# Kernel optimization log

Measured on AMD Instinct MI355X. Metric: run time of the kernel, lower is better.

The kernel has to match this reference:

```python
import jax, jax.numpy as jnp
import numpy as np

B, L, N = 8, 5, 4096
RADIUS, K = 0.7, 32
SPATIAL_STRIDE = 16
TK, TSTRIDE = 3, 2  # temporal kernel / stride; temporal_padding=[1,1] replicate
DIM, DEPTH, HEADS, DIM_HEAD, MLP_DIM, OUT_DIM = 512, 5, 8, 64, 1024, 1088
INNER = HEADS * DIM_HEAD
N_ANCH = 64
NTOT = N + N_ANCH
M = NTOT // SPATIAL_STRIDE  # spatial anchors per output frame


def setup_inputs() -> dict:
    key = jax.random.key(0)
    ks = list(jax.random.split(key, 16))
    s = 0.02
    p = {}
    p["points"] = jax.random.uniform(ks[0], (B, L, N, 3), jnp.float32, -1.0, 1.0)
    p["conv_d_w"] = jax.random.normal(ks[1], (DIM, 4), jnp.float32) * s
    p["conv_f_w"] = jax.random.normal(ks[2], (DIM, 3), jnp.float32) * s
    p["pos_w"] = jax.random.normal(ks[3], (DIM, 4), jnp.float32) * s
    p["pos_b"] = jnp.zeros((DIM,), jnp.float32)
    p["ln1_g"] = jnp.ones((DEPTH, DIM)); p["ln1_b"] = jnp.zeros((DEPTH, DIM))
    p["qkv_w"] = jax.random.normal(ks[4], (DEPTH, DIM, 3 * INNER), jnp.float32) * s
    p["attn_out_w"] = jax.random.normal(ks[5], (DEPTH, INNER, DIM), jnp.float32) * s
    p["attn_out_b"] = jnp.zeros((DEPTH, DIM))
    p["ln2_g"] = jnp.ones((DEPTH, DIM)); p["ln2_b"] = jnp.zeros((DEPTH, DIM))
    p["ff1_w"] = jax.random.normal(ks[6], (DEPTH, DIM, MLP_DIM), jnp.float32) * s
    p["ff1_b"] = jnp.zeros((DEPTH, MLP_DIM))
    p["ff2_w"] = jax.random.normal(ks[7], (DEPTH, MLP_DIM, DIM), jnp.float32) * s
    p["ff2_b"] = jnp.zeros((DEPTH, DIM))
    p["head_ln_g"] = jnp.ones((DIM,)); p["head_ln_b"] = jnp.zeros((DIM,))
    p["head1_w"] = jax.random.normal(ks[8], (DIM, MLP_DIM), jnp.float32) * s
    p["head1_b"] = jnp.zeros((MLP_DIM,))
    p["head2_w"] = jax.random.normal(ks[9], (MLP_DIM, OUT_DIM), jnp.float32) * s
    p["head2_b"] = jnp.zeros((OUT_DIM,))
    return p


def _layer_norm(x, g, b, eps=1e-5):
    mu = jnp.mean(x, -1, keepdims=True)
    var = jnp.mean((x - mu) ** 2, -1, keepdims=True)
    return (x - mu) * jax.lax.rsqrt(var + eps) * g + b


def _anchor_grid():
    lin = jnp.linspace(-1.5, 1.5, 4)
    gx, gy, gz = jnp.meshgrid(lin, lin, lin, indexing="ij")
    return jnp.stack([gx.ravel(), gy.ravel(), gz.ravel()], -1)  # (64,3)


def _fps(pts, m):
    # furthest point sampling, pts (N,3) -> (m,) int32, first pick is index 0 (pointnet2 semantics)
    def step(carry, _):
        dist, last = carry
        d = jnp.sum((pts - pts[last]) ** 2, -1)
        dist = jnp.minimum(dist, d)
        return (dist, jnp.argmax(dist).astype(jnp.int32)), last
    init = (jnp.full((pts.shape[0],), 1e10, pts.dtype), jnp.int32(0))
    _, idx = jax.lax.scan(step, init, None, length=m)
    return idx


def _ball_query(anchors, pts, radius, k):
    # first k point indices within radius of each anchor; pad with first hit (0 if none)
    d2 = jnp.sum((anchors[:, None, :] - pts[None, :, :]) ** 2, -1)  # (M,N)
    n = pts.shape[0]
    cand = jnp.where(d2 < radius * radius, jnp.arange(n, dtype=jnp.int32), n)
    neg_topk, _ = jax.lax.top_k(-cand, k)  # k smallest indices, ascending
    idx = -neg_topk
    first = idx[:, :1]
    idx = jnp.where(idx == n, first, idx)
    return jnp.where(idx == n, 0, idx)


def _forward(points, conv_d_w, conv_f_w, pos_w, pos_b, ln1_g, ln1_b, qkv_w,
             attn_out_w, attn_out_b, ln2_g, ln2_b, ff1_w, ff1_b, ff2_w, ff2_b,
             head_ln_g, head_ln_b, head1_w, head1_b, head2_w, head2_b):
    anch = _anchor_grid()  # (64,3)
    pts = jnp.concatenate(
        [points[..., :3], jnp.broadcast_to(anch, (B, L, N_ANCH, 3))], axis=2)  # (B,L,NTOT,3)
    # replicate temporal padding [1,1]
    frames = jnp.concatenate([pts[:, :1], pts, pts[:, -1:]], axis=1)  # (B,L+2,NTOT,3)

    trad = (TK - 1) // 2
    nT = L + 2
    gather = jax.vmap(lambda p, i: p[i])
    out_xyz, out_feat = [], []
    for t in range(trad, nT - trad, TSTRIDE):
        f_t = frames[:, t]                                   # (B,NTOT,3)
        a_idx = jax.vmap(lambda p: _fps(p, M))(f_t)          # (B,M)
        a_xyz = gather(f_t, a_idx)                           # (B,M,3)
        feats_w = []
        for i in range(t - trad, t + trad + 1):
            nb = frames[:, i]                                # (B,NTOT,3)
            idx = jax.vmap(lambda a, p: _ball_query(a, p, RADIUS, K))(a_xyz, nb)  # (B,M,K)
            grouped = gather(nb, idx)                        # (B,M,K,3)
            disp = grouped - a_xyz[:, :, None, :]
            tdisp = jnp.full((B, M, K, 1), float(i - t), disp.dtype)
            disp4 = jnp.concatenate([disp, tdisp], -1)       # (B,M,K,4)
            # conv_f(features) + conv_d(displacement); features fed in are the xyz themselves
            feat = (jnp.einsum("bmkc,dc->bmkd", grouped, conv_f_w)
                    + jnp.einsum("bmkc,dc->bmkd", disp4, conv_d_w))
            feats_w.append(jnp.max(feat, axis=2))            # spatial max -> (B,M,DIM)
        out_feat.append(jnp.max(jnp.stack(feats_w, 0), axis=0))  # temporal max
        out_xyz.append(a_xyz)

    nF = len(out_xyz)
    xyzs = jnp.stack(out_xyz, 1)                             # (B,nF,M,3)
    feats = jnp.stack(out_feat, 1).reshape(B, nF * M, DIM)
    tcol = jnp.broadcast_to(
        jnp.arange(1, nF + 1, dtype=xyzs.dtype)[None, :, None, None], (B, nF, M, 1))
    xyzts = jnp.concatenate([xyzs, tcol], -1).reshape(B, nF * M, 4)
    x = jnp.einsum("bnc,dc->bnd", xyzts, pos_w) + pos_b + feats  # (B,T,DIM); emb_relu=False

    scale = DIM_HEAD ** -0.5
    for l in range(DEPTH):
        xn = _layer_norm(x, ln1_g[l], ln1_b[l])
        q, k, v = jnp.split(xn @ qkv_w[l], 3, axis=-1)
        rs = lambda a: a.reshape(B, -1, HEADS, DIM_HEAD)
        q, k, v = rs(q), rs(k), rs(v)
        att = jax.nn.softmax(jnp.einsum("bqhd,bkhd->bhqk", q, k) * scale, axis=-1)
        o = jnp.einsum("bhqk,bkhd->bqhd", att, v).reshape(B, -1, INNER)
        x = x + o @ attn_out_w[l] + attn_out_b[l]
        xn = _layer_norm(x, ln2_g[l], ln2_b[l])
        x = x + jax.nn.gelu(xn @ ff1_w[l] + ff1_b[l], approximate=False) @ ff2_w[l] + ff2_b[l]

    x = jnp.max(x, axis=1)                                   # (B,DIM)
    x = _layer_norm(x, head_ln_g, head_ln_b)
    x = jax.nn.gelu(x @ head1_w + head1_b, approximate=False) @ head2_w + head2_b
    x = x.reshape(B, 1, OUT_DIM // 64, 64)
    x = jax.nn.softmax(x, axis=-1)
    return x @ anch                                          # (B,1,J,3)


def reference(points, conv_d_w, conv_f_w, pos_w, pos_b, ln1_g, ln1_b, qkv_w,
              attn_out_w, attn_out_b, ln2_g, ln2_b, ff1_w, ff1_b, ff2_w, ff2_b,
              head_ln_g, head_ln_b, head1_w, head1_b, head2_w, head2_b):
    return _forward(points, conv_d_w, conv_f_w, pos_w, pos_b, ln1_g, ln1_b, qkv_w,
                    attn_out_w, attn_out_b, ln2_g, ln2_b, ff1_w, ff1_b, ff2_w, ff2_b,
                    head_ln_g, head_ln_b, head1_w, head1_b, head2_w, head2_b)
```

## Files before the change

kernel.cpp:

```cpp
#include <hip/hip_runtime.h>
#include <hip/hip_bf16.h>
#include <cstddef>

#define BB 8
#define LL 5
#define NN 4096
#define NANCH 64
#define NPTS 4160
#define MM 260
#define NFRAME 3
#define SSEQ 780
#define DIMC 512
#define NHEAD 8
#define DHEAD 64
#define MLPD 1024
#define OUTD 1088
#define NROWS 6240
#define VPITCH 784
#define WBUFSZ 2097152

typedef __attribute__((ext_vector_type(8))) short s16x8;
typedef __attribute__((ext_vector_type(4))) float fx4;
typedef unsigned short ushort_t;
typedef unsigned int uint_t;

__device__ __forceinline__ float sqdist_rn(float x1, float y1, float z1,
                                           float x2, float y2, float z2) {
    float dx = __fsub_rn(x1, x2);
    float dy = __fsub_rn(y1, y2);
    float dz = __fsub_rn(z1, z2);
    return __fadd_rn(__fadd_rn(__fmul_rn(dx, dx), __fmul_rn(dy, dy)), __fmul_rn(dz, dz));
}

__device__ __forceinline__ float gelu_exact(float v) {
    return 0.5f * v * (1.0f + erff(v * 0.70710678118654752440f));
}

__device__ __forceinline__ uint_t bf16rn(float f) {
    uint_t u = __float_as_uint(f);
    return (u + 0x7FFFu + ((u >> 16) & 1u)) >> 16;
}
__device__ __forceinline__ void split2(float f, ushort_t& h, ushort_t& l) {
    uint_t hb = bf16rn(f);
    h = (ushort_t)hb;
    float fh = __uint_as_float(hb << 16);
    l = (ushort_t)bf16rn(f - fh);
}

typedef __attribute__((address_space(3))) unsigned int as3u;
typedef const __attribute__((address_space(1))) unsigned int as1u;
__device__ __forceinline__ void gload16(const ushort_t* g, ushort_t* l) {
    __builtin_amdgcn_global_load_lds((as1u*)g, (as3u*)l, 16, 0, 0);
}

template <int CTRL>
__device__ __forceinline__ int dpp_mov(int v) {
    return __builtin_amdgcn_update_dpp(0, v, CTRL, 0xF, 0xF, true);
}
#define DPP_STEP_F(op, v, ctrl) v = op(v, __int_as_float(dpp_mov<ctrl>(__float_as_int(v))))
__device__ __forceinline__ float wave_max_bcast(float v) {
    DPP_STEP_F(fmaxf, v, 0x111); DPP_STEP_F(fmaxf, v, 0x112);
    DPP_STEP_F(fmaxf, v, 0x114); DPP_STEP_F(fmaxf, v, 0x118);
    DPP_STEP_F(fmaxf, v, 0x142); DPP_STEP_F(fmaxf, v, 0x143);
    return __int_as_float(__builtin_amdgcn_readlane(__float_as_int(v), 63));
}
__device__ __forceinline__ float faddf(float a, float b) { return a + b; }
__device__ __forceinline__ float wave_sum_bcast(float v) {
    DPP_STEP_F(faddf, v, 0x111); DPP_STEP_F(faddf, v, 0x112);
    DPP_STEP_F(faddf, v, 0x114); DPP_STEP_F(faddf, v, 0x118);
    DPP_STEP_F(faddf, v, 0x142); DPP_STEP_F(faddf, v, 0x143);
    return __int_as_float(__builtin_amdgcn_readlane(__float_as_int(v), 63));
}
__device__ __forceinline__ float row16_maxf(float v) {
    DPP_STEP_F(fmaxf, v, 0x111); DPP_STEP_F(fmaxf, v, 0x112);
    DPP_STEP_F(fmaxf, v, 0x114); DPP_STEP_F(fmaxf, v, 0x118);
    return __int_as_float(__builtin_amdgcn_readlane(__float_as_int(v), 15));
}

__device__ __forceinline__ void wsplit_tile(
    int bid, int tid, int nthr,
    const float* __restrict__ qkvw, const float* __restrict__ projw,
    const float* __restrict__ ff1w, const float* __restrict__ ff2w,
    ushort_t* __restrict__ th, ushort_t* __restrict__ tl,
    float (*T)[33]) {
    const float* src; int K, N; size_t dst;
    if (bid < 768)       { src = qkvw;  K = 512;  N = 1536; dst = 0;       }
    else if (bid < 1024) { src = projw; K = 512;  N = 512;  dst = 786432;  bid -= 768;  }
    else if (bid < 1536) { src = ff1w;  K = 512;  N = 1024; dst = 1048576; bid -= 1024; }
    else                 { src = ff2w;  K = 1024; N = 512;  dst = 1572864; bid -= 1536; }
    int ntn = N >> 5;
    int tn = bid % ntn, tk = bid / ntn;
    int n0 = tn * 32, k0 = tk * 32;
    for (int e = tid; e < 1024; e += nthr) {
        int r = e >> 5, c = e & 31;
        T[r][c] = src[(size_t)(k0 + r) * N + n0 + c];
    }
    __syncthreads();
    for (int e = tid; e < 1024; e += nthr) {
        int r = e >> 5, c = e & 31;
        ushort_t h, l;
        split2(T[c][r], h, l);
        th[dst + (size_t)(n0 + r) * K + k0 + c] = h;
        tl[dst + (size_t)(n0 + r) * K + k0 + c] = l;
    }
}

__global__ __launch_bounds__(256) void build_pts_kernel(const float* __restrict__ points,
                                                        float* __restrict__ pts) {
    int i = blockIdx.x * 256 + threadIdx.x;
    if (i >= BB * LL * NPTS) return;
    int n = i % NPTS;
    int bl = i / NPTS;
    if (n < NN) {
        const float* src = points + ((size_t)bl * NN + n) * 3;
        pts[(size_t)i * 3 + 0] = src[0];
        pts[(size_t)i * 3 + 1] = src[1];
        pts[(size_t)i * 3 + 2] = src[2];
    } else {
        int j = n - NN;
        int ix = j >> 4, iy = (j >> 2) & 3, iz = j & 3;
        pts[(size_t)i * 3 + 0] = -1.5f + (float)ix;
        pts[(size_t)i * 3 + 1] = -1.5f + (float)iy;
        pts[(size_t)i * 3 + 2] = -1.5f + (float)iz;
    }
}

__global__ __launch_bounds__(1024) void fps_ws_kernel(
    const float* __restrict__ pts, float* __restrict__ axyz,
    const float* __restrict__ qkvw, const float* __restrict__ projw,
    const float* __restrict__ ff1w, const float* __restrict__ ff2w,
    ushort_t* __restrict__ th, ushort_t* __restrict__ tl) {
    __shared__ __align__(16) char smem[50432];
    int bid = blockIdx.x;
    int tid = threadIdx.x;
    if (bid >= 24) {
        wsplit_tile(bid - 24, tid, 1024, qkvw, projw, ff1w, ff2w, th, tl,
                    (float(*)[33])smem);
        return;
    }
    float* sx = (float*)smem;
    float* sy = sx + NPTS;
    float* sz = sy + NPTS;
    float* redv = sz + NPTS;
    int* redi = (int*)(redv + 32);

    int b = bid / 3, f = bid % 3;
    const float* P = pts + (size_t)(b * LL + 2 * f) * NPTS * 3;
    int lane = tid & 63, wid = tid >> 6;
    int start = tid < 64 ? 5 * tid : 320 + 4 * (tid - 64);
    int cnt = tid < 64 ? 5 : 4;
    float px[5], py[5], pz[5], dist[5];
#pragma unroll
    for (int j = 0; j < 5; j++) {
        if (j < cnt) {
            int n = start + j;
            float gx = P[(size_t)n * 3 + 0];
            float gy = P[(size_t)n * 3 + 1];
            float gz = P[(size_t)n * 3 + 2];
            px[j] = gx; py[j] = gy; pz[j] = gz;
            sx[n] = gx; sy[n] = gy; sz[n] = gz;
            dist[j] = 1e10f;
        } else {
            px[j] = 0.f; py[j] = 0.f; pz[j] = 0.f;
            dist[j] = -1.0f;
        }
    }
    __syncthreads();
    float ax = sx[0], ay = sy[0], az = sz[0];
    float* out = axyz + (size_t)bid * MM * 3;
    for (int m = 0; m < MM; m++) {
        if (tid == 0) { out[m * 3 + 0] = ax; out[m * 3 + 1] = ay; out[m * 3 + 2] = az; }
        float bv = -1.0f;
#pragma unroll
        for (int j = 0; j < 4; j++) {
            float d = sqdist_rn(px[j], py[j], pz[j], ax, ay, az);
            float dj = fminf(dist[j], d);
            dist[j] = dj;
            bv = fmaxf(bv, dj);
        }
        if (cnt == 5) {
            float d = sqdist_rn(px[4], py[4], pz[4], ax, ay, az);
            float dj = fminf(dist[4], d);
            dist[4] = dj;
            bv = fmaxf(bv, dj);
        }
        float wmv = wave_max_bcast(bv);
        unsigned long long mk = __ballot(bv == wmv);
        int srcl = __ffsll(mk) - 1;
        int fn = start;
#pragma unroll
        for (int j = 4; j >= 0; j--)
            if (dist[j] == wmv) fn = start + j;
        int wn = __builtin_amdgcn_readlane(fn, srcl);
        int par = (m & 1) * 16;
        if (lane == 0) { redv[par + wid] = wmv; redi[par + wid] = wn; }
        __syncthreads();
        float cv = redv[par + (lane & 15)];
        int ci = redi[par + (lane & 15)];
        float bw = row16_maxf(cv);
        unsigned long long mk2 = __ballot(cv == bw);
        int w16 = __ffsll(mk2) - 1;
        int bn = __builtin_amdgcn_readlane(ci, w16);
        ax = sx[bn]; ay = sy[bn]; az = sz[bn];
    }
}

__global__ __launch_bounds__(64) void group_conv_kernel(
    const float* __restrict__ pts, const float* __restrict__ axyz,
    const float* __restrict__ conv_d_w, const float* __restrict__ conv_f_w,
    const float* __restrict__ pos_w, const float* __restrict__ pos_b,
    float* __restrict__ x) {
    int gid = blockIdx.x;
    int b = gid / SSEQ;
    int rem = gid % SSEQ;
    int f = rem / MM;
    int lane = threadIdx.x;
    const float* A = axyz + (size_t)gid * 3;
    float ax = A[0], ay = A[1], az = A[2];

    float cf0[8], cf1[8], cf2[8], cd0[8], cd1[8], cd2[8], cd3[8], fmx[8];
#pragma unroll
    for (int c = 0; c < 8; c++) {
        int d = lane + 64 * c;
        cf0[c] = conv_f_w[d * 3 + 0];
        cf1[c] = conv_f_w[d * 3 + 1];
        cf2[c] = conv_f_w[d * 3 + 2];
        cd0[c] = conv_d_w[d * 4 + 0];
        cd1[c] = conv_d_w[d * 4 + 1];
        cd2[c] = conv_d_w[d * 4 + 2];
        cd3[c] = conv_d_w[d * 4 + 3];
        fmx[c] = -INFINITY;
    }
    __shared__ int nbr[32];
    __shared__ float gxs[32], gys[32], gzs[32];
    const float R2 = 0.49000000953674316f;

    for (int wi = 0; wi < 3; wi++) {
        int l = 2 * f + wi - 1;
        l = l < 0 ? 0 : (l > 4 ? 4 : l);
        const float* P = pts + (size_t)(b * LL + l) * NPTS * 3;
        int cnt = 0;
        for (int base = 0; base < NPTS && cnt < 32; base += 64) {
            int n = base + lane;
            float d2 = sqdist_rn(P[(size_t)n * 3], P[(size_t)n * 3 + 1], P[(size_t)n * 3 + 2],
                                 ax, ay, az);
            bool hit = d2 < R2;
            unsigned long long mk = __ballot(hit);
            int rank = (int)__popcll(mk & (((unsigned long long)1 << lane) - 1ull));
            if (hit && (cnt + rank) < 32) nbr[cnt + rank] = n;
            cnt += (int)__popcll(mk);
        }
        __syncthreads();
        int eff = cnt < 32 ? cnt : 32;
        if (lane < 32) {
            int idx = (eff == 0) ? 0 : (lane < eff ? nbr[lane] : nbr[0]);
            gxs[lane] = P[(size_t)idx * 3 + 0];
            gys[lane] = P[(size_t)idx * 3 + 1];
            gzs[lane] = P[(size_t)idx * 3 + 2];
        }
        __syncthreads();
        float tf = (float)(wi - 1);
        for (int k = 0; k < 32; k++) {
            float gx = gxs[k], gy = gys[k], gz = gzs[k];
            float dx = gx - ax, dy = gy - ay, dz = gz - az;
#pragma unroll
            for (int c = 0; c < 8; c++) {
                float v = gx * cf0[c] + gy * cf1[c] + gz * cf2[c] +
                          dx * cd0[c] + dy * cd1[c] + dz * cd2[c] + tf * cd3[c];
                fmx[c] = fmaxf(fmx[c], v);
            }
        }
        __syncthreads();
    }
    float tcol = (float)(f + 1);
#pragma unroll
    for (int c = 0; c < 8; c++) {
        int d = lane + 64 * c;
        float pos = ax * pos_w[d * 4 + 0] + ay * pos_w[d * 4 + 1] +
                    az * pos_w[d * 4 + 2] + tcol * pos_w[d * 4 + 3] + pos_b[d];
        x[(size_t)gid * DIMC + d] = fmx[c] + pos;
    }
}

__global__ __launch_bounds__(64) void ln_kernel(const float* __restrict__ x,
                                                const float* __restrict__ g,
                                                const float* __restrict__ b,
                                                ushort_t* __restrict__ yh,
                                                ushort_t* __restrict__ yl) {
    int r = blockIdx.x;
    int lane = threadIdx.x;
    const float* xr = x + (size_t)r * DIMC;
    float4 v0 = *(const float4*)(xr + lane * 8);
    float4 v1 = *(const float4*)(xr + lane * 8 + 4);
    float s = v0.x + v0.y + v0.z + v0.w + v1.x + v1.y + v1.z + v1.w;
    s = wave_sum_bcast(s);
    float mean = s * (1.0f / 512.0f);
    float dv[8];
    dv[0] = v0.x - mean; dv[1] = v0.y - mean; dv[2] = v0.z - mean; dv[3] = v0.w - mean;
    dv[4] = v1.x - mean; dv[5] = v1.y - mean; dv[6] = v1.z - mean; dv[7] = v1.w - mean;
    float sq = 0.f;
#pragma unroll
    for (int c = 0; c < 8; c++) sq += dv[c] * dv[c];
    sq = wave_sum_bcast(sq);
    float var = sq * (1.0f / 512.0f);
    float inv = 1.0f / sqrtf(var + 1e-5f);
    int d = lane * 8;
    ushort_t hs[8], ls[8];
#pragma unroll
    for (int c = 0; c < 8; c++) {
        float v = dv[c] * inv * g[d + c] + b[d + c];
        split2(v, hs[c], ls[c]);
    }
    uint4 hv, lv;
    hv.x = hs[0] | ((uint_t)hs[1] << 16); hv.y = hs[2] | ((uint_t)hs[3] << 16);
    hv.z = hs[4] | ((uint_t)hs[5] << 16); hv.w = hs[6] | ((uint_t)hs[7] << 16);
    lv.x = ls[0] | ((uint_t)ls[1] << 16); lv.y = ls[2] | ((uint_t)ls[3] << 16);
    lv.z = ls[4] | ((uint_t)ls[5] << 16); lv.w = ls[6] | ((uint_t)ls[7] << 16);
    *(uint4*)(yh + (size_t)r * DIMC + d) = hv;
    *(uint4*)(yl + (size_t)r * DIMC + d) = lv;
}

#define BK 32

template <int BN, int EPI>
__global__ __launch_bounds__(256) void gemm_mfma(
    const ushort_t* __restrict__ Ahg, const ushort_t* __restrict__ Alg,
    const ushort_t* __restrict__ Bhg, const ushort_t* __restrict__ Blg,
    const float* __restrict__ bias, const float* __restrict__ R,
    float* __restrict__ C, ushort_t* __restrict__ Ch, ushort_t* __restrict__ Cl,
    ushort_t* __restrict__ Vh, ushort_t* __restrict__ Vl,
    int M, int N, int K) {
    const int WN = BN / 2, NT = WN / 16;
    __shared__ __align__(16) ushort_t Ah[128 * BK];
    __shared__ __align__(16) ushort_t Al[128 * BK];
    __shared__ __align__(16) ushort_t Bh[BN * BK];
    __shared__ __align__(16) ushort_t Bl[BN * BK];
    int tid = threadIdx.x;
    int lane = tid & 63, w = tid >> 6;
    int wm = w & 1, wn = w >> 1;
    int quad = lane >> 4, l15 = lane & 15;
    int m0 = blockIdx.y * 128, n0 = blockIdx.x * BN;

    int sr = lane >> 2;
    int sc = lane & 3;
    int kq = ((sc ^ ((sr >> 1) & 3)) << 3);

    int aoff[2];
#pragma unroll
    for (int i = 0; i < 2; i++) {
        int g = w + 4 * i;
        int row = m0 + g * 16 + sr; if (row >= M) row = M - 1;
        aoff[i] = row * K + kq;
    }
    int boff[BN == 128 ? 2 : 1];
    if (BN == 128) {
#pragma unroll
        for (int i = 0; i < 2; i++) {
            int g = w + 4 * i;
            boff[i] = (n0 + g * 16 + sr) * K + kq;
        }
    } else {
        boff[0] = (n0 + w * 16 + sr) * K + kq;
    }

    fx4 acc[4][NT];
#pragma unroll
    for (int mi = 0; mi < 4; mi++)
#pragma unroll
        for (int nj = 0; nj < NT; nj++) acc[mi][nj] = (fx4){0.f, 0.f, 0.f, 0.f};

    int rsw = (l15 >> 1) & 3;
    int aro = (64 * wm + l15) * BK + ((quad ^ rsw) << 3);
    int bro = (WN * wn + l15) * BK + ((quad ^ rsw) << 3);

    for (int k0 = 0; k0 < K; k0 += BK) {
#pragma unroll
        for (int i = 0; i < 2; i++) {
            int g = w + 4 * i;
            gload16(Ahg + aoff[i] + k0, &Ah[g * 16 * BK]);
            gload16(Alg + aoff[i] + k0, &Al[g * 16 * BK]);
        }
        if (BN == 128) {
#pragma unroll
            for (int i = 0; i < 2; i++) {
                int g = w + 4 * i;
                gload16(Bhg + boff[i] + k0, &Bh[g * 16 * BK]);
                gload16(Blg + boff[i] + k0, &Bl[g * 16 * BK]);
            }
        } else {
            gload16(Bhg + boff[0] + k0, &Bh[w * 16 * BK]);
            gload16(Blg + boff[0] + k0, &Bl[w * 16 * BK]);
        }
        __syncthreads();

        s16x8 bf[NT][2];
#pragma unroll
        for (int nj = 0; nj < NT; nj++) {
            bf[nj][0] = *(const s16x8*)&Bh[bro + 16 * nj * BK];
            bf[nj][1] = *(const s16x8*)&Bl[bro + 16 * nj * BK];
        }
#pragma unroll
        for (int mi = 0; mi < 4; mi++) {
            s16x8 aH = *(const s16x8*)&Ah[aro + 16 * mi * BK];
            s16x8 aL = *(const s16x8*)&Al[aro + 16 * mi * BK];
#pragma unroll
            for (int nj = 0; nj < NT; nj++) {
                acc[mi][nj] = __builtin_amdgcn_mfma_f32_16x16x32_bf16(aH, bf[nj][0], acc[mi][nj], 0, 0, 0);
                acc[mi][nj] = __builtin_amdgcn_mfma_f32_16x16x32_bf16(aH, bf[nj][1], acc[mi][nj], 0, 0, 0);
                acc[mi][nj] = __builtin_amdgcn_mfma_f32_16x16x32_bf16(aL, bf[nj][0], acc[mi][nj], 0, 0, 0);
            }
        }
        __syncthreads();
    }
#pragma unroll
    for (int mi = 0; mi < 4; mi++) {
#pragma unroll
        for (int r = 0; r < 4; r++) {
            int row = m0 + 64 * wm + 16 * mi + quad * 4 + r;
            if (row < M) {
#pragma unroll
                for (int nj = 0; nj < NT; nj++) {
                    int col = n0 + WN * wn + 16 * nj + l15;
                    float v = acc[mi][nj][r];
                    if (EPI == 0) {
                        C[(size_t)row * N + col] = v;
                    } else if (EPI == 3) {
                        C[(size_t)row * N + col] = v + bias[col] + R[(size_t)row * N + col];
                    } else if (EPI == 2) {
                        float gv = gelu_exact(v + bias[col]);
                        ushort_t h, l;
                        split2(gv, h, l);
                        Ch[(size_t)row * N + col] = h;
                        Cl[(size_t)row * N + col] = l;
                    } else if (EPI == 5) {
                        ushort_t h, l;
                        split2(v, h, l);
                        if (col < 1024) {
                            Ch[(size_t)row * 1024 + col] = h;
                            Cl[(size_t)row * 1024 + col] = l;
                        } else {
                            int bb = row / SSEQ, key = row % SSEQ;
                            int hh = (col - 1024) >> 6, dd = (col - 1024) & 63;
                            size_t vo = ((size_t)((bb * 8 + hh) * 64 + dd)) * VPITCH + key;
                            Vh[vo] = h;
                            Vl[vo] = l;
                        }
                    }
                }
            }
        }
    }
}

#define AP 72

__global__ __launch_bounds__(256, 2) void attn_mfma_kernel(
    const ushort_t* __restrict__ qkh, const ushort_t* __restrict__ qkl,
    const ushort_t* __restrict__ vth, const ushort_t* __restrict__ vtl,
    ushort_t* __restrict__ oh, ushort_t* __restrict__ ol,
    const float* __restrict__ nqkvw, const float* __restrict__ nprojw,
    const float* __restrict__ nff1w, const float* __restrict__ nff2w,
    ushort_t* __restrict__ nth, ushort_t* __restrict__ ntl) {
    __shared__ __align__(16) char smem[73728];
    if (blockIdx.x >= 13) {
        int widx = (blockIdx.x - 13) * 64 + blockIdx.y * 8 + blockIdx.z;
        wsplit_tile(widx, threadIdx.x, 256, nqkvw, nprojw, nff1w, nff2w,
                    nth, ntl, (float(*)[33])smem);
        return;
    }
    ushort_t* Qh  = (ushort_t*)smem;
    ushort_t* Ql  = Qh + 64 * AP;
    ushort_t* Kh  = Ql + 64 * AP;
    ushort_t* Kl  = Kh + 64 * AP;
    ushort_t* Vth = Kl + 64 * AP;
    ushort_t* Vtl = Vth + 64 * AP;
    ushort_t* Ph  = Vtl + 64 * AP;
    ushort_t* Pl  = Ph + 64 * AP;

    int qt = blockIdx.x, h = blockIdx.y, b = blockIdx.z;
    int tid = threadIdx.x;
    int lane = tid & 63, w = tid >> 6;
    int quad = lane >> 4, l15 = lane & 15;
    int bh = b * 8 + h;

    int q0 = qt * 64;
    int nq = SSEQ - q0; if (nq > 64) nq = 64;

#pragma unroll
    for (int i = 0; i < 2; i++) {
        int t = tid + 256 * i;
        int row = t >> 3, c = (t & 7) * 8;
        int gq = q0 + (row < nq ? row : nq - 1);
        size_t go = (size_t)(b * SSEQ + gq) * 1024 + h * 64 + c;
        *(uint4*)&Qh[row * AP + c] = *(const uint4*)(qkh + go);
        *(uint4*)&Ql[row * AP + c] = *(const uint4*)(qkl + go);
    }

    fx4 accO[4];
#pragma unroll
    for (int dj = 0; dj < 4; dj++) accO[dj] = (fx4){0.f, 0.f, 0.f, 0.f};
    fx4 accL = (fx4){0.f, 0.f, 0.f, 0.f};

    s16x8 ones;
#pragma unroll
    for (int j = 0; j < 8; j++) ones[j] = (short)16256;

    for (int kt = 0; kt < 13; kt++) {
        int k0 = kt * 64;
        int nk = SSEQ - k0; if (nk > 64) nk = 64;
        __syncthreads();
#pragma unroll
        for (int i = 0; i < 2; i++) {
            int t = tid + 256 * i;
            int row = t >> 3, c = (t & 7) * 8;
            int gk = k0 + (row < nk ? row : nk - 1);
            size_t go = (size_t)(b * SSEQ + gk) * 1024 + h * 64 + c;
            *(uint4*)&Kh[row * AP + c] = *(const uint4*)(qkh + go + 512);
            *(uint4*)&Kl[row * AP + c] = *(const uint4*)(qkl + go + 512);
            size_t vo = ((size_t)(bh * 64 + row)) * VPITCH + k0 + c;
            *(uint4*)&Vth[row * AP + c] = *(const uint4*)(vth + vo);
            *(uint4*)&Vtl[row * AP + c] = *(const uint4*)(vtl + vo);
        }
        __syncthreads();

        fx4 accS[4];
#pragma unroll
        for (int nj = 0; nj < 4; nj++) accS[nj] = (fx4){0.f, 0.f, 0.f, 0.f};
#pragma unroll
        for (int ks = 0; ks < 2; ks++) {
            s16x8 aH = *(const s16x8*)&Qh[(16 * w + l15) * AP + 32 * ks + quad * 8];
            s16x8 aL = *(const s16x8*)&Ql[(16 * w + l15) * AP + 32 * ks + quad * 8];
#pragma unroll
            for (int nj = 0; nj < 4; nj++) {
                s16x8 bH = *(const s16x8*)&Kh[(16 * nj + l15) * AP + 32 * ks + quad * 8];
                s16x8 bL = *(const s16x8*)&Kl[(16 * nj + l15) * AP + 32 * ks + quad * 8];
                accS[nj] = __builtin_amdgcn_mfma_f32_16x16x32_bf16(aH, bH, accS[nj], 0, 0, 0);
                accS[nj] = __builtin_amdgcn_mfma_f32_16x16x32_bf16(aH, bL, accS[nj], 0, 0, 0);
                accS[nj] = __builtin_amdgcn_mfma_f32_16x16x32_bf16(aL, bH, accS[nj], 0, 0, 0);
            }
        }
#pragma unroll
        for (int nj = 0; nj < 4; nj++) {
            int key = 16 * nj + l15;
            bool valid = key < nk;
#pragma unroll
            for (int r = 0; r < 4; r++) {
                float s = accS[nj][r] * 0.125f;
                float p = valid ? __expf(s) : 0.f;
                ushort_t hh, ll;
                split2(p, hh, ll);
                int qrow = 16 * w + quad * 4 + r;
                Ph[qrow * AP + key] = hh;
                Pl[qrow * AP + key] = ll;
            }
        }
#pragma unroll
        for (int ks = 0; ks < 2; ks++) {
            s16x8 aPh = *(const s16x8*)&Ph[(16 * w + l15) * AP + 32 * ks + quad * 8];
            s16x8 aPl = *(const s16x8*)&Pl[(16 * w + l15) * AP + 32 * ks + quad * 8];
            accL = __builtin_amdgcn_mfma_f32_16x16x32_bf16(aPh, ones, accL, 0, 0, 0);
            accL = __builtin_amdgcn_mfma_f32_16x16x32_bf16(aPl, ones, accL, 0, 0, 0);
#pragma unroll
            for (int dj = 0; dj < 4; dj++) {
                s16x8 bVh = *(const s16x8*)&Vth[(16 * dj + l15) * AP + 32 * ks + quad * 8];
                s16x8 bVl = *(const s16x8*)&Vtl[(16 * dj + l15) * AP + 32 * ks + quad * 8];
                accO[dj] = __builtin_amdgcn_mfma_f32_16x16x32_bf16(aPh, bVh, accO[dj], 0, 0, 0);
                accO[dj] = __builtin_amdgcn_mfma_f32_16x16x32_bf16(aPh, bVl, accO[dj], 0, 0, 0);
                accO[dj] = __builtin_amdgcn_mfma_f32_16x16x32_bf16(aPl, bVh, accO[dj], 0, 0, 0);
            }
        }
    }
#pragma unroll
    for (int r = 0; r < 4; r++) {
        int lq = 16 * w + quad * 4 + r;
        if (lq < nq) {
            float inv = 1.0f / accL[r];
            size_t base = (size_t)(b * SSEQ + q0 + lq) * DIMC + h * 64 + l15;
#pragma unroll
            for (int dj = 0; dj < 4; dj++) {
                ushort_t hh, ll;
                split2(accO[dj][r] * inv, hh, ll);
                oh[base + 16 * dj] = hh;
                ol[base + 16 * dj] = ll;
            }
        }
    }
}

__global__ __launch_bounds__(512) void pool_max_kernel(const float* __restrict__ x,
                                                       float* __restrict__ partial) {
    int c = blockIdx.x;
    int bb = blockIdx.y;
    int d = threadIdx.x;
    const float* xb = x + ((size_t)(bb * SSEQ + c * 60)) * DIMC + d;
    float m = -INFINITY;
#pragma unroll 4
    for (int s = 0; s < 60; s++) m = fmaxf(m, xb[(size_t)s * DIMC]);
    partial[((size_t)bb * 13 + c) * DIMC + d] = m;
}

__global__ __launch_bounds__(512) void pool_ln_kernel(const float* __restrict__ partial,
                                                      const float* __restrict__ g,
                                                      const float* __restrict__ b,
                                                      float* __restrict__ out) {
    int bb = blockIdx.x;
    int d = threadIdx.x;
    const float* pb = partial + (size_t)bb * 13 * DIMC + d;
    float m = -INFINITY;
#pragma unroll
    for (int c = 0; c < 13; c++) m = fmaxf(m, pb[(size_t)c * DIMC]);
    __shared__ float col[512];
    __shared__ float red[512];
    col[d] = m;
    red[d] = m;
    __syncthreads();
    for (int s = 256; s > 0; s >>= 1) {
        if (d < s) red[d] += red[d + s];
        __syncthreads();
    }
    float mean = red[0] * (1.0f / 512.0f);
    __syncthreads();
    float dv = col[d] - mean;
    red[d] = dv * dv;
    __syncthreads();
    for (int s = 256; s > 0; s >>= 1) {
        if (d < s) red[d] += red[d + s];
        __syncthreads();
    }
    float var = red[0] * (1.0f / 512.0f);
    float inv = 1.0f / sqrtf(var + 1e-5f);
    out[(size_t)bb * DIMC + d] = dv * inv * g[d] + b[d];
}

__global__ __launch_bounds__(256) void head1_kernel(const float* __restrict__ in,
                                                    const float* __restrict__ W,
                                                    const float* __restrict__ bias,
                                                    float* __restrict__ out) {
    int g = blockIdx.x, bb = blockIdx.y;
    int tid = threadIdx.x;
    int c = tid & 63, ks = tid >> 6;
    int col = g * 64 + c;
    __shared__ float xr[512];
    xr[tid] = in[(size_t)bb * 512 + tid];
    xr[tid + 256] = in[(size_t)bb * 512 + tid + 256];
    __syncthreads();
    float acc = 0.f;
    const float* Wc = W + col;
    for (int k = ks * 128; k < ks * 128 + 128; k++)
        acc += xr[k] * Wc[(size_t)k * MLPD];
    __shared__ float red[256];
    red[tid] = acc;
    __syncthreads();
    if (ks == 0) {
        float v = red[c] + red[c + 64] + red[c + 128] + red[c + 192] + bias[col];
        out[(size_t)bb * MLPD + col] = gelu_exact(v);
    }
}

__global__ __launch_bounds__(256) void head2_kernel(const float* __restrict__ in,
                                                    const float* __restrict__ W,
                                                    const float* __restrict__ bias,
                                                    float* __restrict__ out) {
    int g = blockIdx.x, bb = blockIdx.y;
    int tid = threadIdx.x;
    int c = tid & 63, ks = tid >> 6;
    int col = g * 64 + c;
    __shared__ float xr[1024];
    xr[tid] = in[(size_t)bb * 1024 + tid];
    xr[tid + 256] = in[(size_t)bb * 1024 + tid + 256];
    xr[tid + 512] = in[(size_t)bb * 1024 + tid + 512];
    xr[tid + 768] = in[(size_t)bb * 1024 + tid + 768];
    __syncthreads();
    float acc = 0.f;
    const float* Wc = W + col;
    for (int k = ks * 256; k < ks * 256 + 256; k++)
        acc += xr[k] * Wc[(size_t)k * OUTD];
    __shared__ float red[256];
    red[tid] = acc;
    __syncthreads();
    if (ks == 0) {
        out[(size_t)bb * OUTD + col] = red[c] + red[c + 64] + red[c + 128] + red[c + 192] + bias[col];
    }
}

__global__ __launch_bounds__(64) void smax_anchor_kernel(const float* __restrict__ h2,
                                                         float* __restrict__ out) {
    int bb = blockIdx.x / 17;
    int gcol = blockIdx.x % 17;
    int j = threadIdx.x;
    float v = h2[(size_t)bb * OUTD + gcol * 64 + j];
    float mx = wave_max_bcast(v);
    float p = expf(v - mx);
    float sum = wave_sum_bcast(p);
    int ix = j >> 4, iy = (j >> 2) & 3, iz = j & 3;
    float sx = wave_sum_bcast(p * (-1.5f + (float)ix));
    float sy = wave_sum_bcast(p * (-1.5f + (float)iy));
    float sz = wave_sum_bcast(p * (-1.5f + (float)iz));
    if (j == 0) {
        float* o = out + ((size_t)bb * 17 + gcol) * 3;
        o[0] = sx / sum;
        o[1] = sy / sum;
        o[2] = sz / sum;
    }
}

extern "C" void kernel_launch(void* const* d_in, const int* in_sizes, int n_in,
                              void* d_out, int out_size, void* d_ws, size_t ws_size,
                              hipStream_t stream) {
    const float* points     = (const float*)d_in[0];
    const float* conv_d_w   = (const float*)d_in[1];
    const float* conv_f_w   = (const float*)d_in[2];
    const float* pos_w      = (const float*)d_in[3];
    const float* pos_b      = (const float*)d_in[4];
    const float* ln1_g      = (const float*)d_in[5];
    const float* ln1_b      = (const float*)d_in[6];
    const float* qkv_w      = (const float*)d_in[7];
    const float* attn_out_w = (const float*)d_in[8];
    const float* attn_out_b = (const float*)d_in[9];
    const float* ln2_g      = (const float*)d_in[10];
    const float* ln2_b      = (const float*)d_in[11];
    const float* ff1_w      = (const float*)d_in[12];
    const float* ff1_b      = (const float*)d_in[13];
    const float* ff2_w      = (const float*)d_in[14];
    const float* ff2_b      = (const float*)d_in[15];
    const float* head_ln_g  = (const float*)d_in[16];
    const float* head_ln_b  = (const float*)d_in[17];
    const float* head1_w    = (const float*)d_in[18];
    const float* head1_b    = (const float*)d_in[19];
    const float* head2_w    = (const float*)d_in[20];
    const float* head2_b    = (const float*)d_in[21];

    float* ws = (float*)d_ws;
    float* pts    = ws;
    float* axyz   = pts + 499200;
    float* xbuf   = axyz + 18720;
    float* qkvreg = xbuf + 3194880;
    float* pooled = qkvreg + 9601024;
    float* h1     = pooled + 4096;
    float* h2     = h1 + 8192;
    float* fend   = h2 + 8704;
    ushort_t* qkh = (ushort_t*)qkvreg;
    ushort_t* qkl = qkh + 6389760;
    ushort_t* vth = qkl + 6389760;
    ushort_t* vtl = vth + 3211264;
    ushort_t* us   = (ushort_t*)fend;
    ushort_t* xnh  = us;
    ushort_t* xnl  = xnh + 3194880;
    ushort_t* atth = xnl + 3194880;
    ushort_t* attl = atth + 3194880;
    ushort_t* ffhh = attl + 3194880;
    ushort_t* ffhl = ffhh + 6389760;
    ushort_t* wbh  = ffhl + 6389760;
    ushort_t* wbl  = wbh + 2 * WBUFSZ;
    float* ppart = qkvreg;

    build_pts_kernel<<<650, 256, 0, stream>>>(points, pts);
    fps_ws_kernel<<<24 + 2048, 1024, 0, stream>>>(
        pts, axyz, qkv_w, attn_out_w, ff1_w, ff2_w, wbh, wbl);
    group_conv_kernel<<<NROWS, 64, 0, stream>>>(pts, axyz, conv_d_w, conv_f_w,
                                                pos_w, pos_b, xbuf);
    const int MB = (NROWS + 127) / 128;
    for (int l = 0; l < 5; l++) {
        ushort_t* wth = wbh + (size_t)(l & 1) * WBUFSZ;
        ushort_t* wtl = wbl + (size_t)(l & 1) * WBUFSZ;
        ushort_t* nth = wbh + (size_t)((l + 1) & 1) * WBUFSZ;
        ushort_t* ntl = wbl + (size_t)((l + 1) & 1) * WBUFSZ;
        int ln2off = l * 512;
        ln_kernel<<<NROWS, 64, 0, stream>>>(xbuf, ln1_g + ln2off, ln1_b + ln2off, xnh, xnl);
        gemm_mfma<128, 5><<<dim3(1536 / 128, MB), 256, 0, stream>>>(
            xnh, xnl, wth, wtl, nullptr, nullptr, nullptr, qkh, qkl, vth, vtl,
            NROWS, 1536, 512);
        int lnx = l + 1;
        attn_mfma_kernel<<<dim3(l < 4 ? 45 : 13, NHEAD, BB), 256, 0, stream>>>(
            qkh, qkl, vth, vtl, atth, attl,
            l < 4 ? qkv_w + (size_t)lnx * 512 * 1536 : nullptr,
            l < 4 ? attn_out_w + (size_t)lnx * 512 * 512 : nullptr,
            l < 4 ? ff1_w + (size_t)lnx * 512 * 1024 : nullptr,
            l < 4 ? ff2_w + (size_t)lnx * 1024 * 512 : nullptr,
            nth, ntl);
        gemm_mfma<64, 3><<<dim3(512 / 64, MB), 256, 0, stream>>>(
            atth, attl, wth + 786432, wtl + 786432, attn_out_b + ln2off, xbuf,
            xbuf, nullptr, nullptr, nullptr, nullptr, NROWS, 512, 512);
        ln_kernel<<<NROWS, 64, 0, stream>>>(xbuf, ln2_g + ln2off, ln2_b + ln2off, xnh, xnl);
        gemm_mfma<128, 2><<<dim3(1024 / 128, MB), 256, 0, stream>>>(
            xnh, xnl, wth + 1048576, wtl + 1048576, ff1_b + l * 1024, nullptr,
            nullptr, ffhh, ffhl, nullptr, nullptr, NROWS, 1024, 512);
        gemm_mfma<64, 3><<<dim3(512 / 64, MB), 256, 0, stream>>>(
            ffhh, ffhl, wth + 1572864, wtl + 1572864, ff2_b + ln2off, xbuf,
            xbuf, nullptr, nullptr, nullptr, nullptr, NROWS, 512, 1024);
    }
    pool_max_kernel<<<dim3(13, BB), 512, 0, stream>>>(xbuf, ppart);
    pool_ln_kernel<<<BB, 512, 0, stream>>>(ppart, head_ln_g, head_ln_b, pooled);
    head1_kernel<<<dim3(16, BB), 256, 0, stream>>>(pooled, head1_w, head1_b, h1);
    head2_kernel<<<dim3(17, BB), 256, 0, stream>>>(h1, head2_w, head2_b, h2);
    smax_anchor_kernel<<<BB * 17, 64, 0, stream>>>(h2, (float*)d_out);
}
```

Before: 1.987 ms.

## Shrink FPS block to 4 waves, prefetch next tiles in GEMM and attention

The FPS kernel now runs with 256 threads, each holding 16-17 points in registers. Each thread tracks its best index inline, and the cross-wave reduction is a scalar scan over 4 entries, so the per-iteration barrier covers fewer waves. The split-bf16 GEMM now issues the next K-tile's global-to-LDS loads right after the current fragments are read into registers, overlapping them with the MFMAs. The attention kernel prefetches the next K/V tile into registers while computing on the current one. These changes cost more registers per thread, which may lower occupancy.

```diff
diff --git a/kernel.cpp b/kernel.cpp
--- a/kernel.cpp
+++ b/kernel.cpp
@@ -70,11 +70,6 @@
     DPP_STEP_F(faddf, v, 0x114); DPP_STEP_F(faddf, v, 0x118);
     DPP_STEP_F(faddf, v, 0x142); DPP_STEP_F(faddf, v, 0x143);
     return __int_as_float(__builtin_amdgcn_readlane(__float_as_int(v), 63));
-}
-__device__ __forceinline__ float row16_maxf(float v) {
-    DPP_STEP_F(fmaxf, v, 0x111); DPP_STEP_F(fmaxf, v, 0x112);
-    DPP_STEP_F(fmaxf, v, 0x114); DPP_STEP_F(fmaxf, v, 0x118);
-    return __int_as_float(__builtin_amdgcn_readlane(__float_as_int(v), 15));
 }
 
 __device__ __forceinline__ void wsplit_tile(
@@ -125,16 +120,16 @@
     }
 }
 
-__global__ __launch_bounds__(1024) void fps_ws_kernel(
+__global__ __launch_bounds__(256) void fps_ws_kernel(
     const float* __restrict__ pts, float* __restrict__ axyz,
     const float* __restrict__ qkvw, const float* __restrict__ projw,
     const float* __restrict__ ff1w, const float* __restrict__ ff2w,
     ushort_t* __restrict__ th, ushort_t* __restrict__ tl) {
-    __shared__ __align__(16) char smem[50432];
+    __shared__ __align__(16) char smem[50048];
     int bid = blockIdx.x;
     int tid = threadIdx.x;
     if (bid >= 24) {
-        wsplit_tile(bid - 24, tid, 1024, qkvw, projw, ff1w, ff2w, th, tl,
+        wsplit_tile(bid - 24, tid, 256, qkvw, projw, ff1w, ff2w, th, tl,
                     (float(*)[33])smem);
         return;
     }
@@ -142,28 +137,34 @@
     float* sy = sx + NPTS;
     float* sz = sy + NPTS;
     float* redv = sz + NPTS;
-    int* redi = (int*)(redv + 32);
+    int* redi = (int*)(redv + 8);
 
     int b = bid / 3, f = bid % 3;
     const float* P = pts + (size_t)(b * LL + 2 * f) * NPTS * 3;
     int lane = tid & 63, wid = tid >> 6;
-    int start = tid < 64 ? 5 * tid : 320 + 4 * (tid - 64);
-    int cnt = tid < 64 ? 5 : 4;
-    float px[5], py[5], pz[5], dist[5];
-#pragma unroll
-    for (int j = 0; j < 5; j++) {
-        if (j < cnt) {
-            int n = start + j;
-            float gx = P[(size_t)n * 3 + 0];
-            float gy = P[(size_t)n * 3 + 1];
-            float gz = P[(size_t)n * 3 + 2];
-            px[j] = gx; py[j] = gy; pz[j] = gz;
-            sx[n] = gx; sy[n] = gy; sz[n] = gz;
-            dist[j] = 1e10f;
-        } else {
-            px[j] = 0.f; py[j] = 0.f; pz[j] = 0.f;
-            dist[j] = -1.0f;
-        }
+    int start = tid < 64 ? 17 * tid : 1088 + 16 * (tid - 64);
+    float px[17], py[17], pz[17], dist[17];
+#pragma unroll
+    for (int j = 0; j < 16; j++) {
+        int n = start + j;
+        float gx = P[(size_t)n * 3 + 0];
+        float gy = P[(size_t)n * 3 + 1];
+        float gz = P[(size_t)n * 3 + 2];
+        px[j] = gx; py[j] = gy; pz[j] = gz;
+        sx[n] = gx; sy[n] = gy; sz[n] = gz;
+        dist[j] = 1e10f;
+    }
+    if (tid < 64) {
+        int n = start + 16;
+        float gx = P[(size_t)n * 3 + 0];
+        float gy = P[(size_t)n * 3 + 1];
+        float gz = P[(size_t)n * 3 + 2];
+        px[16] = gx; py[16] = gy; pz[16] = gz;
+        sx[n] = gx; sy[n] = gy; sz[n] = gz;
+        dist[16] = 1e10f;
+    } else {
+        px[16] = 0.f; py[16] = 0.f; pz[16] = 0.f;
+        dist[16] = -1.0f;
     }
     __syncthreads();
     float ax = sx[0], ay = sy[0], az = sz[0];
@@ -171,36 +172,35 @@
     for (int m = 0; m < MM; m++) {
         if (tid == 0) { out[m * 3 + 0] = ax; out[m * 3 + 1] = ay; out[m * 3 + 2] = az; }
         float bv = -1.0f;
-#pragma unroll
-        for (int j = 0; j < 4; j++) {
+        int bjn = start;
+#pragma unroll
+        for (int j = 0; j < 16; j++) {
             float d = sqdist_rn(px[j], py[j], pz[j], ax, ay, az);
             float dj = fminf(dist[j], d);
             dist[j] = dj;
-            bv = fmaxf(bv, dj);
-        }
-        if (cnt == 5) {
-            float d = sqdist_rn(px[4], py[4], pz[4], ax, ay, az);
-            float dj = fminf(dist[4], d);
-            dist[4] = dj;
-            bv = fmaxf(bv, dj);
+            if (dj > bv) { bv = dj; bjn = start + j; }
+        }
+        if (tid < 64) {
+            float d = sqdist_rn(px[16], py[16], pz[16], ax, ay, az);
+            float dj = fminf(dist[16], d);
+            dist[16] = dj;
+            if (dj > bv) { bv = dj; bjn = start + 16; }
         }
         float wmv = wave_max_bcast(bv);
         unsigned long long mk = __ballot(bv == wmv);
         int srcl = __ffsll(mk) - 1;
-        int fn = start;
-#pragma unroll
-        for (int j = 4; j >= 0; j--)
-            if (dist[j] == wmv) fn = start + j;
-        int wn = __builtin_amdgcn_readlane(fn, srcl);
-        int par = (m & 1) * 16;
+        int wn = __builtin_amdgcn_readlane(bjn, srcl);
+        int par = (m & 1) * 4;
         if (lane == 0) { redv[par + wid] = wmv; redi[par + wid] = wn; }
         __syncthreads();
-        float cv = redv[par + (lane & 15)];
-        int ci = redi[par + (lane & 15)];
-        float bw = row16_maxf(cv);
-        unsigned long long mk2 = __ballot(cv == bw);
-        int w16 = __ffsll(mk2) - 1;
-        int bn = __builtin_amdgcn_readlane(ci, w16);
+        float b0 = redv[par + 0], b1 = redv[par + 1];
+        float b2 = redv[par + 2], b3 = redv[par + 3];
+        int i0 = redi[par + 0], i1 = redi[par + 1];
+        int i2 = redi[par + 2], i3 = redi[par + 3];
+        float bb = b0; int bn = i0;
+        if (b1 > bb) { bb = b1; bn = i1; }
+        if (b2 > bb) { bb = b2; bn = i2; }
+        if (b3 > bb) { bb = b3; bn = i3; }
         ax = sx[bn]; ay = sy[bn]; az = sz[bn];
     }
 }
@@ -373,27 +373,30 @@
     int aro = (64 * wm + l15) * BK + ((quad ^ rsw) << 3);
     int bro = (WN * wn + l15) * BK + ((quad ^ rsw) << 3);
 
-    for (int k0 = 0; k0 < K; k0 += BK) {
+    auto stage = [&](int kk) {
 #pragma unroll
         for (int i = 0; i < 2; i++) {
             int g = w + 4 * i;
-            gload16(Ahg + aoff[i] + k0, &Ah[g * 16 * BK]);
-            gload16(Alg + aoff[i] + k0, &Al[g * 16 * BK]);
+            gload16(Ahg + aoff[i] + kk, &Ah[g * 16 * BK]);
+            gload16(Alg + aoff[i] + kk, &Al[g * 16 * BK]);
         }
         if (BN == 128) {
 #pragma unroll
             for (int i = 0; i < 2; i++) {
                 int g = w + 4 * i;
-                gload16(Bhg + boff[i] + k0, &Bh[g * 16 * BK]);
-                gload16(Blg + boff[i] + k0, &Bl[g * 16 * BK]);
+                gload16(Bhg + boff[i] + kk, &Bh[g * 16 * BK]);
+                gload16(Blg + boff[i] + kk, &Bl[g * 16 * BK]);
             }
         } else {
-            gload16(Bhg + boff[0] + k0, &Bh[w * 16 * BK]);
-            gload16(Blg + boff[0] + k0, &Bl[w * 16 * BK]);
-        }
-        __syncthreads();
-
-        s16x8 bf[NT][2];
+            gload16(Bhg + boff[0] + kk, &Bh[w * 16 * BK]);
+            gload16(Blg + boff[0] + kk, &Bl[w * 16 * BK]);
+        }
+    };
+
+    stage(0);
+    for (int k0 = 0; k0 < K; k0 += BK) {
+        __syncthreads();
+        s16x8 af[4][2], bf[NT][2];
 #pragma unroll
         for (int nj = 0; nj < NT; nj++) {
             bf[nj][0] = *(const s16x8*)&Bh[bro + 16 * nj * BK];
@@ -401,16 +404,19 @@
         }
 #pragma unroll
         for (int mi = 0; mi < 4; mi++) {
-            s16x8 aH = *(const s16x8*)&Ah[aro + 16 * mi * BK];
-            s16x8 aL = *(const s16x8*)&Al[aro + 16 * mi * BK];
+            af[mi][0] = *(const s16x8*)&Ah[aro + 16 * mi * BK];
+            af[mi][1] = *(const s16x8*)&Al[aro + 16 * mi * BK];
+        }
+        __syncthreads();
+        if (k0 + BK < K) stage(k0 + BK);
+#pragma unroll
+        for (int mi = 0; mi < 4; mi++)
 #pragma unroll
             for (int nj = 0; nj < NT; nj++) {
-                acc[mi][nj] = __builtin_amdgcn_mfma_f32_16x16x32_bf16(aH, bf[nj][0], acc[mi][nj], 0, 0, 0);
-                acc[mi][nj] = __builtin_amdgcn_mfma_f32_16x16x32_bf16(aH, bf[nj][1], acc[mi][nj], 0, 0, 0);
-                acc[mi][nj] = __builtin_amdgcn_mfma_f32_16x16x32_bf16(aL, bf[nj][0], acc[mi][nj], 0, 0, 0);
+                acc[mi][nj] = __builtin_amdgcn_mfma_f32_16x16x32_bf16(af[mi][0], bf[nj][0], acc[mi][nj], 0, 0, 0);
+                acc[mi][nj] = __builtin_amdgcn_mfma_f32_16x16x32_bf16(af[mi][0], bf[nj][1], acc[mi][nj], 0, 0, 0);
+                acc[mi][nj] = __builtin_amdgcn_mfma_f32_16x16x32_bf16(af[mi][1], bf[nj][0], acc[mi][nj], 0, 0, 0);
             }
-        }
-        __syncthreads();
     }
 #pragma unroll
     for (int mi = 0; mi < 4; mi++) {
@@ -505,23 +511,48 @@
 #pragma unroll
     for (int j = 0; j < 8; j++) ones[j] = (short)16256;
 
+    int c8 = (tid & 7) * 8;
+    int srow = tid >> 3;
+    uint4 rkh[2], rkl[2], rvh[2], rvl[2];
+#pragma unroll
+    for (int i = 0; i < 2; i++) {
+        int row = srow + 32 * i;
+        size_t go = (size_t)(b * SSEQ + row) * 1024 + h * 64 + c8;
+        rkh[i] = *(const uint4*)(qkh + go + 512);
+        rkl[i] = *(const uint4*)(qkl + go + 512);
+        size_t vo = ((size_t)(bh * 64 + row)) * VPITCH + c8;
+        rvh[i] = *(const uint4*)(vth + vo);
+        rvl[i] = *(const uint4*)(vtl + vo);
+    }
+
     for (int kt = 0; kt < 13; kt++) {
         int k0 = kt * 64;
         int nk = SSEQ - k0; if (nk > 64) nk = 64;
         __syncthreads();
 #pragma unroll
         for (int i = 0; i < 2; i++) {
-            int t = tid + 256 * i;
-            int row = t >> 3, c = (t & 7) * 8;
-            int gk = k0 + (row < nk ? row : nk - 1);
-            size_t go = (size_t)(b * SSEQ + gk) * 1024 + h * 64 + c;
-            *(uint4*)&Kh[row * AP + c] = *(const uint4*)(qkh + go + 512);
-            *(uint4*)&Kl[row * AP + c] = *(const uint4*)(qkl + go + 512);
-            size_t vo = ((size_t)(bh * 64 + row)) * VPITCH + k0 + c;
-            *(uint4*)&Vth[row * AP + c] = *(const uint4*)(vth + vo);
-            *(uint4*)&Vtl[row * AP + c] = *(const uint4*)(vtl + vo);
-        }
-        __syncthreads();
+            int row = srow + 32 * i;
+            *(uint4*)&Kh[row * AP + c8] = rkh[i];
+            *(uint4*)&Kl[row * AP + c8] = rkl[i];
+            *(uint4*)&Vth[row * AP + c8] = rvh[i];
+            *(uint4*)&Vtl[row * AP + c8] = rvl[i];
+        }
+        __syncthreads();
+        if (kt < 12) {
+            int k1 = k0 + 64;
+            int nk1 = SSEQ - k1; if (nk1 > 64) nk1 = 64;
+#pragma unroll
+            for (int i = 0; i < 2; i++) {
+                int row = srow + 32 * i;
+                int gk = k1 + (row < nk1 ? row : nk1 - 1);
+                size_t go = (size_t)(b * SSEQ + gk) * 1024 + h * 64 + c8;
+                rkh[i] = *(const uint4*)(qkh + go + 512);
+                rkl[i] = *(const uint4*)(qkl + go + 512);
+                size_t vo = ((size_t)(bh * 64 + row)) * VPITCH + k1 + c8;
+                rvh[i] = *(const uint4*)(vth + vo);
+                rvl[i] = *(const uint4*)(vtl + vo);
+            }
+        }
 
         fx4 accS[4];
 #pragma unroll
@@ -755,7 +786,7 @@
     float* ppart = qkvreg;
 
     build_pts_kernel<<<650, 256, 0, stream>>>(points, pts);
-    fps_ws_kernel<<<24 + 2048, 1024, 0, stream>>>(
+    fps_ws_kernel<<<24 + 2048, 256, 0, stream>>>(
         pts, axyz, qkv_w, attn_out_w, ff1_w, ff2_w, wbh, wbl);
     group_conv_kernel<<<NROWS, 64, 0, stream>>>(pts, axyz, conv_d_w, conv_f_w,
                                                 pos_w, pos_b, xbuf);
```

Result: slower. 2.047 ms (+3.0%).
